# Kernel tuning notes

Measured on AMD Instinct MI355X. Metric: run time of the kernel, lower is better.

## Reference

```python
import jax, jax.numpy as jnp
import numpy as np

B, T, IN, H, L = 64, 1024, 512, 1024, 2
ZO = 0.1  # zoneout prob; eval-mode blend factor


def setup_inputs() -> dict:
    key = jax.random.key(0)
    ks = jax.random.split(key, 9)
    s = 1.0 / np.sqrt(H)  # torch GRUCell uniform init bound

    def w(k, shape):
        return jax.random.uniform(k, shape, jnp.float32, -s, s)

    return dict(
        x=jax.random.normal(ks[0], (B, T, IN), jnp.float32),
        h0=jnp.zeros((L, B, H), jnp.float32),
        w_ih_0=w(ks[1], (3 * H, IN)),
        w_hh_0=w(ks[2], (3 * H, H)),
        b_ih_0=w(ks[3], (3 * H,)),
        b_hh_0=w(ks[4], (3 * H,)),
        w_ih_1=w(ks[5], (3 * H, H)),
        w_hh_1=w(ks[6], (3 * H, H)),
        b_ih_1=w(ks[7], (3 * H,)),
        b_hh_1=w(ks[8], (3 * H,)),
    )


def _gru_cell(inp, h, w_ih, w_hh, b_ih, b_hh):
    # PyTorch GRUCell gate math; gi/gh: [B, 3H]
    gi = inp @ w_ih.T + b_ih
    gh = h @ w_hh.T + b_hh
    i_r, i_z, i_n = jnp.split(gi, 3, axis=-1)
    h_r, h_z, h_n = jnp.split(gh, 3, axis=-1)
    r = jax.nn.sigmoid(i_r + h_r)
    z = jax.nn.sigmoid(i_z + h_z)
    n = jnp.tanh(i_n + r * h_n)
    return (1.0 - z) * n + z * h


def reference(x, h0, w_ih_0, w_hh_0, b_ih_0, b_hh_0, w_ih_1, w_hh_1, b_ih_1, b_hh_1):
    params = [
        (w_ih_0, w_hh_0, b_ih_0, b_hh_0),
        (w_ih_1, w_hh_1, b_ih_1, b_hh_1),
    ]

    def step(h, x_t):  # h: [L,B,H], x_t: [B,IN]
        inp = x_t
        new_hs = []
        for i in range(L):
            nh = _gru_cell(inp, h[i], *params[i])
            # eval-mode zoneout: deterministic blend with prob ZO
            nh = ZO * h[i] + (1.0 - ZO) * nh
            new_hs.append(nh)
            inp = nh  # layer_drop inactive in eval
        return jnp.stack(new_hs), inp

    h_n, outs = jax.lax.scan(step, h0, jnp.swapaxes(x, 0, 1))  # outs: [T,B,H]
    return jnp.swapaxes(outs, 0, 1), h_n
```

## Files before the change

kernel.cpp:

```cpp
#include <hip/hip_runtime.h>


#define Tn 1024
#define Hn 1024
#define INn 512

typedef short s8v __attribute__((ext_vector_type(8)));
typedef float f4v __attribute__((ext_vector_type(4)));
typedef unsigned short us4v __attribute__((ext_vector_type(4)));
typedef unsigned long long ull;

#define WS_XB  0u
#define WS_H0R 67108864u
#define WS_H1R 134217728u
#define WS_MB  167772160u

__device__ __forceinline__ unsigned short f2bf(float f) {
  unsigned int u = __float_as_uint(f);
  u += 0x7fffu + ((u >> 16) & 1u);
  return (unsigned short)(u >> 16);
}

__device__ __forceinline__ s8v pack8(const float* p) {
  float4 a = *(const float4*)p;
  float4 b = *(const float4*)(p + 4);
  s8v r;
  r[0] = (short)f2bf(a.x); r[1] = (short)f2bf(a.y);
  r[2] = (short)f2bf(a.z); r[3] = (short)f2bf(a.w);
  r[4] = (short)f2bf(b.x); r[5] = (short)f2bf(b.y);
  r[6] = (short)f2bf(b.z); r[7] = (short)f2bf(b.w);
  return r;
}

__device__ __forceinline__ void st8c(unsigned short* p, us4v v) {
  union { us4v v; ull u; } c; c.v = v;
  __hip_atomic_store((ull*)p, c.u, __ATOMIC_RELAXED, __HIP_MEMORY_SCOPE_AGENT);
}

__device__ __forceinline__ void stnt16(float* p, f4v v) {
  asm volatile("global_store_dwordx4 %0, %1, off nt" :: "v"(p), "v"(v) : "memory");
}

__device__ __forceinline__ void issue4c(s8v* f, const unsigned short* src,
                                        int kt, int w, int rl, int kg) {
#pragma unroll
  for (int m = 0; m < 4; ++m) {
    const unsigned short* p = src + (size_t)(w * 16 + kt * 2 + (kg >> 1)) * 1024
                              + (m * 16 + rl) * 16 + (kg & 1) * 8;
    asm volatile("global_load_dwordx4 %0, %1, off"
                 : "=v"(f[m]) : "v"(p) : "memory");
  }
}

template<int N> __device__ __forceinline__ void vmwait() {
  asm volatile("s_waitcnt vmcnt(%0)" :: "i"(N) : "memory");
  __builtin_amdgcn_sched_barrier(0);
}

__device__ __forceinline__ void mfma3(f4v (*acc)[4], s8v w0, s8v w1, s8v w2,
                                      const s8v f[4], const int gl) {
#pragma unroll
  for (int m = 0; m < 4; ++m) {
    acc[m][0]  = __builtin_amdgcn_mfma_f32_16x16x32_bf16(w0, f[m], acc[m][0], 0, 0, 0);
    acc[m][1]  = __builtin_amdgcn_mfma_f32_16x16x32_bf16(w1, f[m], acc[m][1], 0, 0, 0);
    acc[m][gl] = __builtin_amdgcn_mfma_f32_16x16x32_bf16(w2, f[m], acc[m][gl], 0, 0, 0);
  }
}

template<int GL>
__device__ __forceinline__ void stream_gemm_deep(f4v (*acc)[4], const s8v (*wgt)[8],
    const unsigned short* src, int w, int rl, int kg) {
  s8v f[6][4];
#pragma unroll
  for (int kt = 0; kt < 6; ++kt) issue4c(f[kt], src, kt, w, rl, kg);
  vmwait<20>(); mfma3(acc, wgt[0][0], wgt[1][0], wgt[2][0], f[0], GL);
  issue4c(f[0], src, 6, w, rl, kg);
  vmwait<20>(); mfma3(acc, wgt[0][1], wgt[1][1], wgt[2][1], f[1], GL);
  issue4c(f[1], src, 7, w, rl, kg);
  vmwait<20>(); mfma3(acc, wgt[0][2], wgt[1][2], wgt[2][2], f[2], GL);
  vmwait<16>(); mfma3(acc, wgt[0][3], wgt[1][3], wgt[2][3], f[3], GL);
  vmwait<12>(); mfma3(acc, wgt[0][4], wgt[1][4], wgt[2][4], f[4], GL);
  vmwait<8>();  mfma3(acc, wgt[0][5], wgt[1][5], wgt[2][5], f[5], GL);
  vmwait<4>();  mfma3(acc, wgt[0][6], wgt[1][6], wgt[2][6], f[0], GL);
  vmwait<0>();  mfma3(acc, wgt[0][7], wgt[1][7], wgt[2][7], f[1], GL);
}

__global__ void cvt_bf16_kernel(const float* __restrict__ src,
                                unsigned short* __restrict__ dst, int n4) {
  int i = blockIdx.x * blockDim.x + threadIdx.x;
  int st = gridDim.x * blockDim.x;
  for (; i < n4; i += st) {
    const float4 v = *(const float4*)(src + 4 * (size_t)i);
    us4v o;
    o[0] = f2bf(v.x); o[1] = f2bf(v.y); o[2] = f2bf(v.z); o[3] = f2bf(v.w);
    *(us4v*)(dst + 4 * (size_t)i) = o;
  }
}

__global__ void init_all(const float* __restrict__ h0in, char* __restrict__ ws) {
  int i = blockIdx.x * blockDim.x + threadIdx.x;
  unsigned short* h0r = (unsigned short*)(ws + WS_H0R);
  unsigned short* h1r = (unsigned short*)(ws + WS_H1R);
  int* MB = (int*)(ws + WS_MB);
  if (i < 65536) {
    int b = i >> 10, h = i & 1023;
    int off = (h >> 4) * 1024 + b * 16 + (h & 15);
    h0r[511 * 65536 + off] = f2bf(h0in[i]);
    h1r[255 * 65536 + off] = f2bf(h0in[65536 + i]);
  }
  if (i < 32768) MB[i] = 0;
}

__device__ __forceinline__ void mb_wait(const int* MB, int r1, int t1,
                                        int r2, int t2, int lane) {
  const int* p1 = MB + (r1 * 64 + lane);
  const int* p2 = MB + (r2 * 64 + lane);
  int tries = 0;
  for (;;) {
    int v1 = __hip_atomic_load(p1, __ATOMIC_RELAXED, __HIP_MEMORY_SCOPE_AGENT);
    int v2 = __hip_atomic_load(p2, __ATOMIC_RELAXED, __HIP_MEMORY_SCOPE_AGENT);
    if (__all(v1 >= t1 && v2 >= t2)) return;
    __builtin_amdgcn_s_sleep(1);
    if (++tries > (1 << 22)) return;
  }
}

__global__ __launch_bounds__(256)
__attribute__((amdgpu_waves_per_eu(1, 1)))
void gru_persist(
    const float* __restrict__ h0in,
    const float* __restrict__ wih0, const float* __restrict__ whh0,
    const float* __restrict__ bih0, const float* __restrict__ bhh0,
    const float* __restrict__ wih1, const float* __restrict__ whh1,
    const float* __restrict__ bih1, const float* __restrict__ bhh1,
    float* __restrict__ out, char* __restrict__ ws)
{
  const unsigned short* xb = (const unsigned short*)(ws + WS_XB);
  unsigned short* h0r = (unsigned short*)(ws + WS_H0R);
  unsigned short* h1r = (unsigned short*)(ws + WS_H1R);
  int* MB = (int*)(ws + WS_MB);

  const int blk = blockIdx.x;
  const int tid = threadIdx.x;

  if (blk >= 128) return;

  const bool isA = blk < 64;
  const int jt = blk & 63, jj = jt * 16;
  const int w = tid >> 6;
  const int lane = tid & 63;
  const int rl = lane & 15, kg = lane >> 4;

  __shared__ float cmb[4][4][64][20];

  const int b = w * 16 + rl;
  const int j0 = jj + kg * 4;

  const float* Wi = isA ? wih0 : wih1;
  const float* Wh = isA ? whh0 : whh1;
  const float* bi = isA ? bih0 : bih1;
  const float* bh = isA ? bhh0 : bhh1;
  s8v wx[3][8], wh_[3][8];
#pragma unroll
  for (int g = 0; g < 3; ++g) {
    if (isA) {
#pragma unroll
      for (int kt = 0; kt < 4; ++kt)
        wx[g][kt] = pack8(Wi + (size_t)(g * 1024 + jj + rl) * INn + w * 128 + kt * 32 + kg * 8);
    } else {
#pragma unroll
      for (int kt = 0; kt < 8; ++kt)
        wx[g][kt] = pack8(Wi + (size_t)(g * 1024 + jj + rl) * Hn + w * 256 + kt * 32 + kg * 8);
    }
#pragma unroll
    for (int kt = 0; kt < 8; ++kt)
      wh_[g][kt] = pack8(Wh + (size_t)(g * 1024 + jj + rl) * Hn + w * 256 + kt * 32 + kg * 8);
  }
  const f4v bir = *(const f4v*)(bi + j0),        bhr = *(const f4v*)(bh + j0);
  const f4v biz = *(const f4v*)(bi + 1024 + j0), bhz = *(const f4v*)(bh + 1024 + j0);
  const f4v bin = *(const f4v*)(bi + 2048 + j0), bhn = *(const f4v*)(bh + 2048 + j0);

  f4v hv = *(const f4v*)(h0in + (isA ? 0u : 65536u) + (size_t)b * Hn + j0);

  for (int s = 0; s < Tn; ++s) {
    s8v bx[4][4];
    if (isA) {
#pragma unroll
      for (int m = 0; m < 4; ++m)
#pragma unroll
        for (int kt = 0; kt < 4; ++kt)
          bx[m][kt] = *(const s8v*)(xb + ((size_t)(m * 16 + rl) * Tn + s) * INn + w * 128 + kt * 32 + kg * 8);
    }
    if (w == 0) {
      if (isA) mb_wait(MB, 0 * 64 + jt, s,     3 * 64 + jt, s - 255, lane);
      else     mb_wait(MB, 1 * 64 + jt, s + 1, 2 * 64 + jt, s,       lane);
    }
    __syncthreads();
    vmwait<0>();

    f4v acc[4][4];
#pragma unroll
    for (int m = 0; m < 4; ++m)
#pragma unroll
      for (int g = 0; g < 4; ++g) acc[m][g] = (f4v){0.f, 0.f, 0.f, 0.f};

    const unsigned short* hsrc = isA ? (h0r + (size_t)((s - 1) & 511) * 65536)
                                     : (h1r + (size_t)((s - 1) & 255) * 65536);
    const unsigned short* asrc = h0r + (size_t)(s & 511) * 65536;

    if (isA) {
#pragma unroll
      for (int kt = 0; kt < 4; ++kt) {
        s8v f4[4] = { bx[0][kt], bx[1][kt], bx[2][kt], bx[3][kt] };
        mfma3(acc, wx[0][kt], wx[1][kt], wx[2][kt], f4, 2);
      }
      stream_gemm_deep<3>(acc, wh_, hsrc, w, rl, kg);
    } else {
      stream_gemm_deep<2>(acc, wx, asrc, w, rl, kg);
      stream_gemm_deep<3>(acc, wh_, hsrc, w, rl, kg);
    }

#pragma unroll
    for (int d = 0; d < 4; ++d) if (d != w)
#pragma unroll
      for (int g = 0; g < 4; ++g) *(f4v*)&cmb[d][w][lane][g * 4] = acc[d][g];
    __syncthreads();
    f4v hsum[4];
#pragma unroll
    for (int g = 0; g < 4; ++g) {
      hsum[g] = acc[w][g];
#pragma unroll
      for (int src = 0; src < 4; ++src) if (src != w) hsum[g] += *(f4v*)&cmb[w][src][lane][g * 4];
    }

    us4v hb4;
#pragma unroll
    for (int rr = 0; rr < 4; ++rr) {
      float hp = hv[rr];
      float rg = 1.f / (1.f + __expf(-(hsum[0][rr] + bir[rr] + bhr[rr])));
      float zg = 1.f / (1.f + __expf(-(hsum[1][rr] + biz[rr] + bhz[rr])));
      float narg = hsum[2][rr] + bin[rr] + rg * (hsum[3][rr] + bhn[rr]);
      float e2 = __expf(2.f * narg);
      float ng = 1.f - 2.f / (e2 + 1.f);
      float nv = (1.f - zg) * ng + zg * hp;
      hv[rr] = 0.1f * hp + 0.9f * nv;
    }
    hb4[0] = f2bf(hv[0]); hb4[1] = f2bf(hv[1]); hb4[2] = f2bf(hv[2]); hb4[3] = f2bf(hv[3]);

    if (isA) {
      st8c(h0r + (size_t)(s & 511) * 65536 + jt * 1024 + b * 16 + kg * 4, hb4);
      if (s == Tn - 1)
        stnt16(out + 67108864u + (size_t)b * Hn + j0, hv);
      vmwait<0>();
    } else {
      st8c(h1r + (size_t)(s & 255) * 65536 + jt * 1024 + b * 16 + kg * 4, hb4);
      stnt16(out + ((size_t)b * Tn + s) * Hn + j0, hv);
      if (s == Tn - 1) {
        stnt16(out + 67108864u + 65536u + (size_t)b * Hn + j0, hv);
        vmwait<0>();
      } else {
        vmwait<1>();
      }
    }
    __syncthreads();
    if (tid < 64) {
      const int g1 = isA ? 0 : 2, g2 = isA ? 1 : 3;
      __hip_atomic_store(MB + ((g1 * 64 + tid) * 64 + jt), s + 1,
                         __ATOMIC_RELAXED, __HIP_MEMORY_SCOPE_AGENT);
      __hip_atomic_store(MB + ((g2 * 64 + tid) * 64 + jt), s + 1,
                         __ATOMIC_RELAXED, __HIP_MEMORY_SCOPE_AGENT);
    }
  }
}

extern "C" void kernel_launch(void* const* d_in, const int* in_sizes, int n_in,
                              void* d_out, int out_size, void* d_ws, size_t ws_size,
                              hipStream_t stream) {
  (void)in_sizes; (void)n_in; (void)out_size; (void)ws_size;
  const float* x    = (const float*)d_in[0];
  const float* h0in = (const float*)d_in[1];
  const float* wih0 = (const float*)d_in[2];
  const float* whh0 = (const float*)d_in[3];
  const float* bih0 = (const float*)d_in[4];
  const float* bhh0 = (const float*)d_in[5];
  const float* wih1 = (const float*)d_in[6];
  const float* whh1 = (const float*)d_in[7];
  const float* bih1 = (const float*)d_in[8];
  const float* bhh1 = (const float*)d_in[9];
  float* out = (float*)d_out;
  char* ws = (char*)d_ws;

  cvt_bf16_kernel<<<2048, 256, 0, stream>>>(x, (unsigned short*)(ws + WS_XB), 33554432 / 4);
  init_all<<<528, 256, 0, stream>>>(h0in, ws);
  gru_persist<<<dim3(256), dim3(256), 0, stream>>>(
      h0in, wih0, whh0, bih0, bhh0, wih1, whh1, bih1, bhh1, out, ws);
}
```

Baseline: 7.756 ms.

## Split layer-B mailbox wait and fuse its two streaming GEMMs into one pipeline

Layer-B blocks now wait only on layer-A's mailbox before prefetching the input activations. They then wait separately on their own layer's hidden-state dependency, which lets the input loads overlap that second wait. The two back-to-back streamed GEMMs (input and recurrent) are merged into one continuous software pipeline, so recurrent-state loads are issued while input MFMAs run and the drain bubble between them disappears. It adds an extra barrier per step and more complex wait ordering, which risks correctness if the mailbox semantics are misread.

```diff
diff --git a/kernel.cpp b/kernel.cpp
--- a/kernel.cpp
+++ b/kernel.cpp
@@ -83,6 +83,28 @@
   vmwait<8>();  mfma3(acc, wgt[0][5], wgt[1][5], wgt[2][5], f[5], GL);
   vmwait<4>();  mfma3(acc, wgt[0][6], wgt[1][6], wgt[2][6], f[0], GL);
   vmwait<0>();  mfma3(acc, wgt[0][7], wgt[1][7], wgt[2][7], f[1], GL);
+}
+
+__device__ __forceinline__ void fused_consume(f4v (*acc)[4],
+    const s8v (*wa)[8], const s8v (*wh)[8],
+    const unsigned short* asrc, const unsigned short* hsrc,
+    s8v (*f)[4], int w, int rl, int kg) {
+  vmwait<20>(); mfma3(acc, wa[0][0], wa[1][0], wa[2][0], f[0], 2); issue4c(f[0], asrc, 6, w, rl, kg);
+  vmwait<20>(); mfma3(acc, wa[0][1], wa[1][1], wa[2][1], f[1], 2); issue4c(f[1], asrc, 7, w, rl, kg);
+  vmwait<20>(); mfma3(acc, wa[0][2], wa[1][2], wa[2][2], f[2], 2); issue4c(f[2], hsrc, 0, w, rl, kg);
+  vmwait<20>(); mfma3(acc, wa[0][3], wa[1][3], wa[2][3], f[3], 2); issue4c(f[3], hsrc, 1, w, rl, kg);
+  vmwait<20>(); mfma3(acc, wa[0][4], wa[1][4], wa[2][4], f[4], 2); issue4c(f[4], hsrc, 2, w, rl, kg);
+  vmwait<20>(); mfma3(acc, wa[0][5], wa[1][5], wa[2][5], f[5], 2); issue4c(f[5], hsrc, 3, w, rl, kg);
+  vmwait<20>(); mfma3(acc, wa[0][6], wa[1][6], wa[2][6], f[0], 2); issue4c(f[0], hsrc, 4, w, rl, kg);
+  vmwait<20>(); mfma3(acc, wa[0][7], wa[1][7], wa[2][7], f[1], 2); issue4c(f[1], hsrc, 5, w, rl, kg);
+  vmwait<20>(); mfma3(acc, wh[0][0], wh[1][0], wh[2][0], f[2], 3); issue4c(f[2], hsrc, 6, w, rl, kg);
+  vmwait<20>(); mfma3(acc, wh[0][1], wh[1][1], wh[2][1], f[3], 3); issue4c(f[3], hsrc, 7, w, rl, kg);
+  vmwait<20>(); mfma3(acc, wh[0][2], wh[1][2], wh[2][2], f[4], 3);
+  vmwait<16>(); mfma3(acc, wh[0][3], wh[1][3], wh[2][3], f[5], 3);
+  vmwait<12>(); mfma3(acc, wh[0][4], wh[1][4], wh[2][4], f[0], 3);
+  vmwait<8>();  mfma3(acc, wh[0][5], wh[1][5], wh[2][5], f[1], 3);
+  vmwait<4>();  mfma3(acc, wh[0][6], wh[1][6], wh[2][6], f[2], 3);
+  vmwait<0>();  mfma3(acc, wh[0][7], wh[1][7], wh[2][7], f[3], 3);
 }
 
 __global__ void cvt_bf16_kernel(const float* __restrict__ src,
@@ -183,21 +205,6 @@
   f4v hv = *(const f4v*)(h0in + (isA ? 0u : 65536u) + (size_t)b * Hn + j0);
 
   for (int s = 0; s < Tn; ++s) {
-    s8v bx[4][4];
-    if (isA) {
-#pragma unroll
-      for (int m = 0; m < 4; ++m)
-#pragma unroll
-        for (int kt = 0; kt < 4; ++kt)
-          bx[m][kt] = *(const s8v*)(xb + ((size_t)(m * 16 + rl) * Tn + s) * INn + w * 128 + kt * 32 + kg * 8);
-    }
-    if (w == 0) {
-      if (isA) mb_wait(MB, 0 * 64 + jt, s,     3 * 64 + jt, s - 255, lane);
-      else     mb_wait(MB, 1 * 64 + jt, s + 1, 2 * 64 + jt, s,       lane);
-    }
-    __syncthreads();
-    vmwait<0>();
-
     f4v acc[4][4];
 #pragma unroll
     for (int m = 0; m < 4; ++m)
@@ -209,6 +216,15 @@
     const unsigned short* asrc = h0r + (size_t)(s & 511) * 65536;
 
     if (isA) {
+      s8v bx[4][4];
+#pragma unroll
+      for (int m = 0; m < 4; ++m)
+#pragma unroll
+        for (int kt = 0; kt < 4; ++kt)
+          bx[m][kt] = *(const s8v*)(xb + ((size_t)(m * 16 + rl) * Tn + s) * INn + w * 128 + kt * 32 + kg * 8);
+      if (w == 0) mb_wait(MB, 0 * 64 + jt, s, 3 * 64 + jt, s - 255, lane);
+      __syncthreads();
+      vmwait<0>();
 #pragma unroll
       for (int kt = 0; kt < 4; ++kt) {
         s8v f4[4] = { bx[0][kt], bx[1][kt], bx[2][kt], bx[3][kt] };
@@ -216,8 +232,15 @@
       }
       stream_gemm_deep<3>(acc, wh_, hsrc, w, rl, kg);
     } else {
-      stream_gemm_deep<2>(acc, wx, asrc, w, rl, kg);
-      stream_gemm_deep<3>(acc, wh_, hsrc, w, rl, kg);
+      if (w == 0) mb_wait(MB, 1 * 64 + jt, s + 1, 1 * 64 + jt, s + 1, lane);
+      __syncthreads();
+      vmwait<0>();
+      s8v f[6][4];
+#pragma unroll
+      for (int t = 0; t < 6; ++t) issue4c(f[t], asrc, t, w, rl, kg);
+      if (w == 0) mb_wait(MB, 2 * 64 + jt, s, 2 * 64 + jt, s, lane);
+      __syncthreads();
+      fused_consume(acc, wx, wh_, asrc, hsrc, f, w, rl, kg);
     }
 
 #pragma unroll
```

Result: slower. 8.883 ms (+14.5%).
